# Optimization experiments

Hardware: AMD Instinct MI355X
Metric: run time of the kernel (lower is better)

Reference implementation:

```python
import jax, jax.numpy as jnp
import numpy as np

CELL_SIDE = 1.0
N_CELL = 4          # self.n
POOL = 8            # pool_size
HIDDEN = 128        # hidden_dim == pooling_dim for type_='social'
GRID = N_CELL * POOL  # 32
N_AGENTS = 1024


def setup_inputs() -> dict:
    key = jax.random.key(0)
    k1, k2, k3, k4, k5 = jax.random.split(key, 5)
    hidden_state = jax.random.normal(k1, (N_AGENTS, HIDDEN), jnp.float32)
    obs1 = jax.random.normal(k2, (N_AGENTS, 2), jnp.float32)
    obs2 = jax.random.normal(k3, (N_AGENTS, 2), jnp.float32)
    fan_in = N_CELL * N_CELL * HIDDEN  # 2048
    W = jax.random.normal(k4, (HIDDEN, fan_in), jnp.float32) / np.float32(np.sqrt(fan_in))
    b = jax.random.normal(k5, (HIDDEN,), jnp.float32) * 0.01
    return {"hidden_state": hidden_state, "obs1": obs1, "obs2": obs2, "W": W, "b": b}


def _social_grid(hidden_state, obs2):
    """Vectorized equivalent of Pooling.social: for each agent i, scatter the
    hidden states of in-range other agents into a 32x32 sub-grid, then 8x8
    sum-pool (lp_pool2d with p=1) down to 4x4."""
    N = obs2.shape[0]
    D = hidden_state.shape[1]
    # relative position of agent j in agent i's fine grid: (N, N, 2)
    rel = (obs2[None, :, :] - obs2[:, None, :]) / (CELL_SIDE / POOL) + GRID / 2.0
    valid = ~jnp.eye(N, dtype=bool)                       # one_cold: exclude self
    nan_x = jnp.isnan(obs2[:, 0])
    valid &= ~nan_x[None, :]                              # other agent NaN mask
    valid &= ~nan_x[:, None]                              # self NaN -> zero grid
    valid &= jnp.all((rel >= 0) & (rel < GRID), axis=-1)  # range mask
    oij = jnp.where(valid[..., None], rel, 0.0).astype(jnp.int32)  # trunc == .long()
    # flat cell index; invalid pairs go to a dump slot GRID*GRID
    oi = jnp.where(valid, oij[..., 0] * GRID + oij[..., 1], GRID * GRID)
    vals = jnp.broadcast_to(hidden_state[None, :, :], (N, N, D))

    def scatter(idx, v):
        # occ[oi] = other_values  (set semantics, as in torch fancy assignment)
        return jnp.zeros((GRID * GRID + 1, D), v.dtype).at[idx].set(v)[: GRID * GRID]

    occ = jax.vmap(scatter)(oi, vals)  # (N, GRID*GRID, D)
    # torch: occ.view(1, -1, 32, 32) reinterprets the (1024, D) buffer as (D, 32, 32)
    occ = occ.reshape(N, D, N_CELL, POOL, N_CELL, POOL).sum(axis=(3, 5))  # sum-pool 8x8
    return occ.reshape(N, D * N_CELL * N_CELL)  # (N, 2048)


def reference(hidden_state, obs1, obs2, W, b):
    grid = _social_grid(hidden_state, obs2)
    return grid @ W.T + b  # embedding Linear(2048 -> 128)
```

## Files before the change

kernel.cpp:

```cpp
#include <hip/hip_runtime.h>
#include <math.h>

#define N_AGENTS 1024
#define HIDDEN   128
#define GRIDSZ   32
#define NCELLS   1024
#define KDIM     2048
#define NSPLIT   16
#define KCHUNK   (KDIM / NSPLIT)
#define BK       16

__global__ __launch_bounds__(256) void k_sh(const float* __restrict__ hidden,
                                            float* __restrict__ Sh) {
    int t = blockIdx.x * 256 + threadIdx.x;
    int j = t >> 2, c = t & 3;
    const float* h = hidden + j * HIDDEN + c * 8;
    float s = 0.f;
#pragma unroll
    for (int u = 0; u < 4; ++u) {
        float4 a = *(const float4*)(h + u * 32);
        float4 b = *(const float4*)(h + u * 32 + 4);
        s += a.x + a.y + a.z + a.w + b.x + b.y + b.z + b.w;
    }
    Sh[t] = s;
}

__global__ __launch_bounds__(256) void k_grid(const float* __restrict__ obs2,
                                              const float4* __restrict__ Sh4,
                                              float4* __restrict__ G4) {
    __shared__ int win[NCELLS];
    __shared__ float2 spos[N_AGENTS];
    __shared__ float4 ssh[N_AGENTS];
    int i = blockIdx.x;
    int tid = threadIdx.x;
    for (int c = tid; c < NCELLS; c += 256) win[c] = -1;
    const float2* o2 = (const float2*)obs2;
    for (int j = tid; j < N_AGENTS; j += 256) {
        spos[j] = o2[j];
        ssh[j] = Sh4[j];
    }
    __syncthreads();
    float2 pi = spos[i];
    if (!isnan(pi.x)) {
        for (int j = tid; j < N_AGENTS; j += 256) {
            float2 pj = spos[j];
            if (j == i || isnan(pj.x)) continue;
            float rx = (pj.x - pi.x) * 8.0f + 16.0f;
            float ry = (pj.y - pi.y) * 8.0f + 16.0f;
            if (rx >= 0.0f && rx < 32.0f && ry >= 0.0f && ry < 32.0f)
                atomicMax(&win[(int)rx * GRIDSZ + (int)ry], j);
        }
    }
    __syncthreads();
    float4* Gr = G4 + (size_t)i * (KDIM / 4);
    for (int p = tid; p < KDIM / 4; p += 256) {
        int w0 = win[2 * p], w1 = win[2 * p + 1];
        float4 v = {0.f, 0.f, 0.f, 0.f};
        if (w0 >= 0) { float4 a = ssh[w0]; v.x += a.x; v.y += a.y; v.z += a.z; v.w += a.w; }
        if (w1 >= 0) { float4 a = ssh[w1]; v.x += a.x; v.y += a.y; v.z += a.z; v.w += a.w; }
        Gr[p] = v;
    }
}

__global__ __launch_bounds__(256) void k_gemm(const float* __restrict__ G,
                                              const float* __restrict__ W,
                                              float* __restrict__ part) {
    __shared__ float Gs[32][BK];
    __shared__ float Ws[BK][HIDDEN];
    int i0 = blockIdx.x * 32;
    int k0 = blockIdx.y * KCHUNK;
    int tid = threadIdx.x;
    int lane5 = tid & 31;
    int mrow = (tid >> 5) * 4;
    float acc[4][4] = {};
    for (int kc = 0; kc < KCHUNK; kc += BK) {
        int kb = k0 + kc;
        if (tid < 128) {
            int m = tid >> 2, q = tid & 3;
            float4 g = *(const float4*)(G + (size_t)(i0 + m) * KDIM + kb + q * 4);
            *(float4*)&Gs[m][q * 4] = g;
        }
        {
            int n = tid >> 1, kk0 = (tid & 1) * 8;
            const float* wp = W + (size_t)n * KDIM + kb + kk0;
            float4 a = *(const float4*)wp;
            float4 bfour = *(const float4*)(wp + 4);
            Ws[kk0 + 0][n] = a.x; Ws[kk0 + 1][n] = a.y;
            Ws[kk0 + 2][n] = a.z; Ws[kk0 + 3][n] = a.w;
            Ws[kk0 + 4][n] = bfour.x; Ws[kk0 + 5][n] = bfour.y;
            Ws[kk0 + 6][n] = bfour.z; Ws[kk0 + 7][n] = bfour.w;
        }
        __syncthreads();
#pragma unroll
        for (int kk = 0; kk < BK; ++kk) {
            float4 wv = *(const float4*)&Ws[kk][lane5 * 4];
#pragma unroll
            for (int m = 0; m < 4; ++m) {
                float gm = Gs[mrow + m][kk];
                acc[m][0] += gm * wv.x;
                acc[m][1] += gm * wv.y;
                acc[m][2] += gm * wv.z;
                acc[m][3] += gm * wv.w;
            }
        }
        __syncthreads();
    }
#pragma unroll
    for (int m = 0; m < 4; ++m) {
        float* o = part + ((size_t)blockIdx.y * N_AGENTS + i0 + mrow + m) * HIDDEN + lane5 * 4;
        *(float4*)o = *(float4*)acc[m];
    }
}

__global__ __launch_bounds__(256) void k_reduce(const float* __restrict__ part,
                                                const float* __restrict__ bias,
                                                float* __restrict__ out) {
    int t = blockIdx.x * 256 + threadIdx.x;
    int h4 = t & (HIDDEN / 4 - 1);
    float4 s = ((const float4*)bias)[h4];
    const float4* p4 = (const float4*)part;
#pragma unroll
    for (int y = 0; y < NSPLIT; ++y) {
        float4 a = p4[(size_t)y * (N_AGENTS * HIDDEN / 4) + t];
        s.x += a.x; s.y += a.y; s.z += a.z; s.w += a.w;
    }
    ((float4*)out)[t] = s;
}

extern "C" void kernel_launch(void* const* d_in, const int* in_sizes, int n_in,
                              void* d_out, int out_size, void* d_ws, size_t ws_size,
                              hipStream_t stream) {
    const float* hidden = (const float*)d_in[0];
    const float* obs2   = (const float*)d_in[2];
    const float* W      = (const float*)d_in[3];
    const float* b      = (const float*)d_in[4];
    float* out = (float*)d_out;

    float* Sh   = (float*)d_ws;
    float* G    = (float*)((char*)d_ws + 16384);
    float* part = (float*)((char*)d_ws + 16384 + 8388608);

    k_sh    <<<16,            256, 0, stream>>>(hidden, Sh);
    k_grid  <<<1024,          256, 0, stream>>>(obs2, (const float4*)Sh, (float4*)G);
    k_gemm  <<<dim3(32, NSPLIT), 256, 0, stream>>>(G, W, part);
    k_reduce<<<128,           256, 0, stream>>>(part, b, out);
}
```

Baseline: 88.75 us.

## Fuse all stages into one cooperative kernel with bf16 MFMA GEMM

Replaces four kernel launches with a single cooperative kernel that uses grid-wide syncs between phases. W and the pooled grid are converted to bf16 and the GEMM runs on MFMA 16x16x32 instructions with a 4-way K split. Each block handles four agents, so the shared position and sum tables are loaded once per four agents. This removes launch overhead and fp32 FMA work, but adds grid-sync costs and bf16 rounding error.

```diff
diff --git a/kernel.cpp b/kernel.cpp
--- a/kernel.cpp
+++ b/kernel.cpp
@@ -1,130 +1,130 @@
 #include <hip/hip_runtime.h>
+#include <hip/hip_cooperative_groups.h>
 #include <math.h>
+
+namespace cg = cooperative_groups;
 
 #define N_AGENTS 1024
 #define HIDDEN   128
 #define GRIDSZ   32
 #define NCELLS   1024
 #define KDIM     2048
-#define NSPLIT   16
-#define KCHUNK   (KDIM / NSPLIT)
-#define BK       16
+#define NBLK     256
+#define NTHR     512
+#define NSPLIT   4
 
-__global__ __launch_bounds__(256) void k_sh(const float* __restrict__ hidden,
-                                            float* __restrict__ Sh) {
-    int t = blockIdx.x * 256 + threadIdx.x;
-    int j = t >> 2, c = t & 3;
-    const float* h = hidden + j * HIDDEN + c * 8;
-    float s = 0.f;
-#pragma unroll
-    for (int u = 0; u < 4; ++u) {
-        float4 a = *(const float4*)(h + u * 32);
-        float4 b = *(const float4*)(h + u * 32 + 4);
-        s += a.x + a.y + a.z + a.w + b.x + b.y + b.z + b.w;
-    }
-    Sh[t] = s;
+typedef __attribute__((ext_vector_type(8))) short short8;
+typedef __attribute__((ext_vector_type(4))) float floatx4;
+
+static __device__ __forceinline__ ushort f2bf(float x) {
+    union { float f; unsigned u; } v; v.f = x;
+    return (ushort)((v.u + 0x7fffu + ((v.u >> 16) & 1u)) >> 16);
 }
 
-__global__ __launch_bounds__(256) void k_grid(const float* __restrict__ obs2,
-                                              const float4* __restrict__ Sh4,
-                                              float4* __restrict__ G4) {
-    __shared__ int win[NCELLS];
+__global__ __launch_bounds__(NTHR, 2) void k_fused(
+        const float* __restrict__ hidden, const float* __restrict__ obs2,
+        const float* __restrict__ W, const float* __restrict__ bias,
+        float* __restrict__ out,
+        float* __restrict__ Sh, ushort* __restrict__ Wb,
+        ushort* __restrict__ Gb, float* __restrict__ part) {
+    cg::grid_group grid = cg::this_grid();
     __shared__ float2 spos[N_AGENTS];
     __shared__ float4 ssh[N_AGENTS];
-    int i = blockIdx.x;
-    int tid = threadIdx.x;
-    for (int c = tid; c < NCELLS; c += 256) win[c] = -1;
-    const float2* o2 = (const float2*)obs2;
-    for (int j = tid; j < N_AGENTS; j += 256) {
-        spos[j] = o2[j];
-        ssh[j] = Sh4[j];
+    __shared__ int win[4][NCELLS];
+
+    const int tid = threadIdx.x;
+    const int gt = blockIdx.x * NTHR + tid;
+
+    {
+        float2 w2 = ((const float2*)W)[gt];
+        ((unsigned*)Wb)[gt] = (unsigned)f2bf(w2.x) | ((unsigned)f2bf(w2.y) << 16);
     }
-    __syncthreads();
-    float2 pi = spos[i];
-    if (!isnan(pi.x)) {
-        for (int j = tid; j < N_AGENTS; j += 256) {
+    if (gt < N_AGENTS * 4) {
+        int j = gt >> 2, c = gt & 3;
+        const float* h = hidden + j * HIDDEN + c * 8;
+        float s = 0.f;
+#pragma unroll
+        for (int u = 0; u < 4; ++u) {
+            float4 a = *(const float4*)(h + u * 32);
+            float4 b = *(const float4*)(h + u * 32 + 4);
+            s += a.x + a.y + a.z + a.w + b.x + b.y + b.z + b.w;
+        }
+        Sh[gt] = s;
+    }
+    grid.sync();
+
+    {
+        const float2* o2 = (const float2*)obs2;
+        const float4* Sh4 = (const float4*)Sh;
+        for (int j = tid; j < N_AGENTS; j += NTHR) {
+            spos[j] = o2[j];
+            ssh[j] = Sh4[j];
+        }
+#pragma unroll
+        for (int a = 0; a < 4; ++a)
+            for (int c = tid; c < NCELLS; c += NTHR)
+                win[a][c] = -1;
+        __syncthreads();
+        const int ibase = blockIdx.x * 4;
+        float2 pi[4];
+#pragma unroll
+        for (int a = 0; a < 4; ++a) pi[a] = spos[ibase + a];
+        for (int j = tid; j < N_AGENTS; j += NTHR) {
             float2 pj = spos[j];
-            if (j == i || isnan(pj.x)) continue;
-            float rx = (pj.x - pi.x) * 8.0f + 16.0f;
-            float ry = (pj.y - pi.y) * 8.0f + 16.0f;
-            if (rx >= 0.0f && rx < 32.0f && ry >= 0.0f && ry < 32.0f)
-                atomicMax(&win[(int)rx * GRIDSZ + (int)ry], j);
-        }
-    }
-    __syncthreads();
-    float4* Gr = G4 + (size_t)i * (KDIM / 4);
-    for (int p = tid; p < KDIM / 4; p += 256) {
-        int w0 = win[2 * p], w1 = win[2 * p + 1];
-        float4 v = {0.f, 0.f, 0.f, 0.f};
-        if (w0 >= 0) { float4 a = ssh[w0]; v.x += a.x; v.y += a.y; v.z += a.z; v.w += a.w; }
-        if (w1 >= 0) { float4 a = ssh[w1]; v.x += a.x; v.y += a.y; v.z += a.z; v.w += a.w; }
-        Gr[p] = v;
-    }
-}
-
-__global__ __launch_bounds__(256) void k_gemm(const float* __restrict__ G,
-                                              const float* __restrict__ W,
-                                              float* __restrict__ part) {
-    __shared__ float Gs[32][BK];
-    __shared__ float Ws[BK][HIDDEN];
-    int i0 = blockIdx.x * 32;
-    int k0 = blockIdx.y * KCHUNK;
-    int tid = threadIdx.x;
-    int lane5 = tid & 31;
-    int mrow = (tid >> 5) * 4;
-    float acc[4][4] = {};
-    for (int kc = 0; kc < KCHUNK; kc += BK) {
-        int kb = k0 + kc;
-        if (tid < 128) {
-            int m = tid >> 2, q = tid & 3;
-            float4 g = *(const float4*)(G + (size_t)(i0 + m) * KDIM + kb + q * 4);
-            *(float4*)&Gs[m][q * 4] = g;
-        }
-        {
-            int n = tid >> 1, kk0 = (tid & 1) * 8;
-            const float* wp = W + (size_t)n * KDIM + kb + kk0;
-            float4 a = *(const float4*)wp;
-            float4 bfour = *(const float4*)(wp + 4);
-            Ws[kk0 + 0][n] = a.x; Ws[kk0 + 1][n] = a.y;
-            Ws[kk0 + 2][n] = a.z; Ws[kk0 + 3][n] = a.w;
-            Ws[kk0 + 4][n] = bfour.x; Ws[kk0 + 5][n] = bfour.y;
-            Ws[kk0 + 6][n] = bfour.z; Ws[kk0 + 7][n] = bfour.w;
-        }
-        __syncthreads();
+            if (isnan(pj.x)) continue;
 #pragma unroll
-        for (int kk = 0; kk < BK; ++kk) {
-            float4 wv = *(const float4*)&Ws[kk][lane5 * 4];
-#pragma unroll
-            for (int m = 0; m < 4; ++m) {
-                float gm = Gs[mrow + m][kk];
-                acc[m][0] += gm * wv.x;
-                acc[m][1] += gm * wv.y;
-                acc[m][2] += gm * wv.z;
-                acc[m][3] += gm * wv.w;
+            for (int a = 0; a < 4; ++a) {
+                if (j == ibase + a) continue;
+                float rx = (pj.x - pi[a].x) * 8.0f + 16.0f;
+                float ry = (pj.y - pi[a].y) * 8.0f + 16.0f;
+                if (rx >= 0.f && rx < 32.f && ry >= 0.f && ry < 32.f)
+                    atomicMax(&win[a][(int)rx * GRIDSZ + (int)ry], j);
             }
         }
         __syncthreads();
+        int p = tid;
+#pragma unroll
+        for (int a = 0; a < 4; ++a) {
+            int w0 = win[a][2 * p], w1 = win[a][2 * p + 1];
+            float4 v = {0.f, 0.f, 0.f, 0.f};
+            if (w0 >= 0) { float4 s = ssh[w0]; v.x += s.x; v.y += s.y; v.z += s.z; v.w += s.w; }
+            if (w1 >= 0) { float4 s = ssh[w1]; v.x += s.x; v.y += s.y; v.z += s.z; v.w += s.w; }
+            ushort4 u;
+            u.x = f2bf(v.x); u.y = f2bf(v.y); u.z = f2bf(v.z); u.w = f2bf(v.w);
+            *(ushort4*)(Gb + (size_t)(ibase + a) * KDIM + 4 * p) = u;
+        }
     }
+    grid.sync();
+
+    {
+        int w = (blockIdx.x << 3) + (tid >> 6);
+        int lane = tid & 63;
+        int mt = w >> 5;
+        int nt = (w >> 2) & 7;
+        int ks = w & 3;
+        int r16 = lane & 15, quad = lane >> 4;
+        const ushort* Ga = Gb + (size_t)(mt * 16 + r16) * KDIM + ks * 512 + quad * 8;
+        const ushort* Wa = Wb + (size_t)(nt * 16 + r16) * KDIM + ks * 512 + quad * 8;
+        floatx4 acc = {0.f, 0.f, 0.f, 0.f};
 #pragma unroll
-    for (int m = 0; m < 4; ++m) {
-        float* o = part + ((size_t)blockIdx.y * N_AGENTS + i0 + mrow + m) * HIDDEN + lane5 * 4;
-        *(float4*)o = *(float4*)acc[m];
+        for (int kb = 0; kb < 16; ++kb) {
+            short8 av = *(const short8*)(Ga + kb * 32);
+            short8 bv = *(const short8*)(Wa + kb * 32);
+            acc = __builtin_amdgcn_mfma_f32_16x16x32_bf16(av, bv, acc, 0, 0, 0);
+        }
+        float* pp = part + ((size_t)(ks * N_AGENTS) + mt * 16 + quad * 4) * HIDDEN + nt * 16 + r16;
+#pragma unroll
+        for (int r = 0; r < 4; ++r) pp[(size_t)r * HIDDEN] = acc[r];
     }
-}
+    grid.sync();
 
-__global__ __launch_bounds__(256) void k_reduce(const float* __restrict__ part,
-                                                const float* __restrict__ bias,
-                                                float* __restrict__ out) {
-    int t = blockIdx.x * 256 + threadIdx.x;
-    int h4 = t & (HIDDEN / 4 - 1);
-    float4 s = ((const float4*)bias)[h4];
-    const float4* p4 = (const float4*)part;
+    {
+        float s = bias[gt & (HIDDEN - 1)];
 #pragma unroll
-    for (int y = 0; y < NSPLIT; ++y) {
-        float4 a = p4[(size_t)y * (N_AGENTS * HIDDEN / 4) + t];
-        s.x += a.x; s.y += a.y; s.z += a.z; s.w += a.w;
+        for (int y = 0; y < NSPLIT; ++y)
+            s += part[(size_t)y * (N_AGENTS * HIDDEN) + gt];
+        out[gt] = s;
     }
-    ((float4*)out)[t] = s;
 }
 
 extern "C" void kernel_launch(void* const* d_in, const int* in_sizes, int n_in,
@@ -136,12 +136,12 @@
     const float* b      = (const float*)d_in[4];
     float* out = (float*)d_out;
 
-    float* Sh   = (float*)d_ws;
-    float* G    = (float*)((char*)d_ws + 16384);
-    float* part = (float*)((char*)d_ws + 16384 + 8388608);
+    float*  Sh   = (float*) d_ws;
+    ushort* Wb   = (ushort*)((char*)d_ws + 65536);
+    ushort* Gb   = (ushort*)((char*)d_ws + (1u << 20));
+    float*  part = (float*) ((char*)d_ws + (5u << 20));
 
-    k_sh    <<<16,            256, 0, stream>>>(hidden, Sh);
-    k_grid  <<<1024,          256, 0, stream>>>(obs2, (const float4*)Sh, (float4*)G);
-    k_gemm  <<<dim3(32, NSPLIT), 256, 0, stream>>>(G, W, part);
-    k_reduce<<<128,           256, 0, stream>>>(part, b, out);
+    void* args[] = {&hidden, &obs2, &W, &b, &out, &Sh, &Wb, &Gb, &part};
+    hipLaunchCooperativeKernel((const void*)k_fused, dim3(NBLK), dim3(NTHR),
+                               args, 0, stream);
 }
```

New measurement: 172.1 us. +93.9%, slower.
